# Kernel optimization log

Hardware: AMD Instinct MI355X
Metric: run time of the kernel (lower is better)

The kernel has to match this reference:

```python
import jax, jax.numpy as jnp
import numpy as np

L, B, D, H = 2048, 2, 1024, 16
HD = D // H
DFF = 4 * D
EPS = 1e-5


def layernorm(x, g, b):
    mu = jnp.mean(x, axis=-1, keepdims=True)
    var = jnp.mean((x - mu) ** 2, axis=-1, keepdims=True)
    return (x - mu) * jax.lax.rsqrt(var + EPS) * g + b


def setup_inputs() -> dict:
    key = jax.random.key(0)
    ks = jax.random.split(key, 12)
    s = 0.02
    return {
        "x": jax.random.normal(ks[0], (L, B, D), jnp.float32),
        "ln1_g": jnp.ones((D,), jnp.float32),
        "ln1_b": jnp.zeros((D,), jnp.float32),
        "w_attn": jax.random.normal(ks[1], (D, 3 * D), jnp.float32) * s,
        "b_attn": jnp.zeros((3 * D,), jnp.float32),
        "w_proj": jax.random.normal(ks[2], (D, D), jnp.float32) * s,
        "b_proj": jnp.zeros((D,), jnp.float32),
        "ln2_g": jnp.ones((D,), jnp.float32),
        "ln2_b": jnp.zeros((D,), jnp.float32),
        "w_fc": jax.random.normal(ks[3], (D, DFF), jnp.float32) * s,
        "b_fc": jnp.zeros((DFF,), jnp.float32),
        "w_out": jax.random.normal(ks[4], (DFF, D), jnp.float32) * s,
        "b_out": jnp.zeros((D,), jnp.float32),
    }


def reference(x, ln1_g, ln1_b, w_attn, b_attn, w_proj, b_proj,
              ln2_g, ln2_b, w_fc, b_fc, w_out, b_out):
    # x: [L, B, D]
    h = layernorm(x, ln1_g, ln1_b)
    qkv = h @ w_attn + b_attn                     # [L, B, 3D]
    qkv = jnp.transpose(qkv, (1, 0, 2))            # [B, L, 3D]
    q, k, v = jnp.split(qkv, 3, axis=-1)

    def split_heads(t):                            # [B, L, D] -> [B, H, L, hd]
        return jnp.transpose(t.reshape(B, L, H, HD), (0, 2, 1, 3))

    q, k, v = split_heads(q), split_heads(k), split_heads(v)
    # present: stack of (key, value), key in [B,H,L,hd] layout (post transpose-back)
    present = jnp.stack((k, v))                    # [2, B, H, L, hd]

    scores = jnp.einsum('bhqd,bhkd->bhqk', q, k) / jnp.sqrt(jnp.float32(HD))
    w = jax.nn.softmax(scores, axis=-1)
    a = jnp.einsum('bhqk,bhkd->bhqd', w, v)        # [B, H, L, hd]
    a = jnp.transpose(a, (0, 2, 1, 3)).reshape(B, L, D)
    a = a @ w_proj + b_proj                        # [B, L, D]
    a = jnp.transpose(a, (1, 0, 2))                # [L, B, D]

    x = x + a
    m = jax.nn.gelu(layernorm(x, ln2_g, ln2_b) @ w_fc + b_fc) @ w_out + b_out
    x = x + m
    return x, present
```

## Files before the change

### kernel.cpp

```cpp
#include <hip/hip_runtime.h>
#include <stdint.h>

#define L_SEQ 2048
#define BATCH 2
#define DIM   1024
#define NH    16
#define HDIM  64
#define DFF_  4096
#define ROWS  (L_SEQ*BATCH)

#define QSCALE 0.18033688011112042f

typedef __attribute__((ext_vector_type(8))) short  bf16x8;
typedef __attribute__((ext_vector_type(4))) float  floatx4;

__device__ __forceinline__ unsigned short f2bf(float f) {
    union { float f; uint32_t u; } x; x.f = f;
    uint32_t r = x.u + 0x7fffu + ((x.u >> 16) & 1u);
    return (unsigned short)(r >> 16);
}
__device__ __forceinline__ float bf2f(unsigned short b) {
    union { uint32_t u; float f; } x; x.u = ((uint32_t)b) << 16;
    return x.f;
}
__device__ __forceinline__ uint32_t fbits(float f) {
    union { float f; uint32_t u; } x; x.f = f; return x.u;
}

__device__ __forceinline__ void load_lds16(const unsigned short* g, unsigned short* l) {
    __builtin_amdgcn_global_load_lds(
        (const __attribute__((address_space(1))) unsigned int*)g,
        (__attribute__((address_space(3))) unsigned int*)l, 16, 0, 0);
}

__global__ __launch_bounds__(256)
void transpose_all(const float* __restrict__ s0, unsigned short* __restrict__ d0,
                   const float* __restrict__ s1, unsigned short* __restrict__ d1,
                   const float* __restrict__ s2, unsigned short* __restrict__ d2,
                   const float* __restrict__ s3, unsigned short* __restrict__ d3)
{
    const int id = blockIdx.x;
    const float* src; unsigned short* dst; int K, N, local;
    if (id < 3072)      { src = s0; dst = d0; K = 1024; N = 3072; local = id; }
    else if (id < 4096) { src = s1; dst = d1; K = 1024; N = 1024; local = id - 3072; }
    else if (id < 8192) { src = s2; dst = d2; K = 1024; N = 4096; local = id - 4096; }
    else                { src = s3; dst = d3; K = 4096; N = 1024; local = id - 8192; }
    const int nN = N >> 5;
    const int bk = (local / nN) * 32, bn = (local % nN) * 32;

    __shared__ float tile[32][36];
    const int t = threadIdx.x;
    const int r = t >> 3, c4 = (t & 7) * 4;
    *(float4*)&tile[r][c4] = *(const float4*)(src + (size_t)(bk + r) * N + bn + c4);
    __syncthreads();
    ushort4 o;
    o.x = f2bf(tile[c4 + 0][r]);
    o.y = f2bf(tile[c4 + 1][r]);
    o.z = f2bf(tile[c4 + 2][r]);
    o.w = f2bf(tile[c4 + 3][r]);
    *(ushort4*)(dst + (size_t)(bn + r) * K + bk + c4) = o;
}

template<int INBF16>
__global__ __launch_bounds__(256)
void ln_rows(const void* __restrict__ xin, const float* __restrict__ g,
             const float* __restrict__ bta, unsigned short* __restrict__ out)
{
    const int row = blockIdx.x;
    const int t = threadIdx.x;
    float4 v;
    if (INBF16) {
        const ushort4 u = ((const ushort4*)((const unsigned short*)xin + (size_t)row * DIM))[t];
        v.x = bf2f(u.x); v.y = bf2f(u.y); v.z = bf2f(u.z); v.w = bf2f(u.w);
    } else {
        v = ((const float4*)((const float*)xin + (size_t)row * DIM))[t];
    }
    float s  = v.x + v.y + v.z + v.w;
    float s2 = v.x*v.x + v.y*v.y + v.z*v.z + v.w*v.w;
#pragma unroll
    for (int d = 1; d < 64; d <<= 1) { s += __shfl_xor(s, d, 64); s2 += __shfl_xor(s2, d, 64); }
    __shared__ float ss[4], ss2[4];
    const int w = t >> 6, lane = t & 63;
    if (lane == 0) { ss[w] = s; ss2[w] = s2; }
    __syncthreads();
    s  = ss[0] + ss[1] + ss[2] + ss[3];
    s2 = ss2[0] + ss2[1] + ss2[2] + ss2[3];
    const float mu   = s * (1.0f / DIM);
    const float var  = s2 * (1.0f / DIM) - mu * mu;
    const float rstd = rsqrtf(var + 1e-5f);
    const float4 gv = ((const float4*)g)[t];
    const float4 bv = ((const float4*)bta)[t];
    ushort4 o;
    o.x = f2bf((v.x - mu) * rstd * gv.x + bv.x);
    o.y = f2bf((v.y - mu) * rstd * gv.y + bv.y);
    o.z = f2bf((v.z - mu) * rstd * gv.z + bv.z);
    o.w = f2bf((v.w - mu) * rstd * gv.w + bv.w);
    *(ushort4*)(out + (size_t)row * DIM + t * 4) = o;
}

template<int GELU, int RESID, int OUTBF16, int MI>
__global__ __launch_bounds__(256)
void gemm_bt(const unsigned short* __restrict__ A,
             const unsigned short* __restrict__ Bt,
             const float* __restrict__ bias,
             const void* __restrict__ resid,
             void* __restrict__ outp,
             int M, int N, int K)
{
    __shared__ unsigned short As[MI * 32 * 32];
    __shared__ unsigned short Bs[128 * 32];
    const int t = threadIdx.x;
    const int w = t >> 6, lane = t & 63;
    const int quad = lane >> 4, l16 = lane & 15;
    const int wm = (w >> 1) * (MI * 16), wn = (w & 1) * 64;
    const int bm = blockIdx.x * (MI * 32), bn = blockIdx.y * 128;

    const int srow = lane >> 2;
    const int scol = (lane & 3) * 8;

    const unsigned short* Ab = A  + (size_t)bm * K;
    const unsigned short* Bb = Bt + (size_t)bn * K;

    floatx4 acc[MI][4] = {};

    for (int kc = 0; kc < K; kc += 32) {
        __syncthreads();
#pragma unroll
        for (int i = 0; i < MI / 2; ++i) {
            const int r0 = (i * 4 + w) * 16;
            load_lds16(Ab + (size_t)(r0 + srow) * K + kc + scol, As + r0 * 32);
        }
#pragma unroll
        for (int i = 0; i < 2; ++i) {
            const int r0 = (i * 4 + w) * 16;
            load_lds16(Bb + (size_t)(r0 + srow) * K + kc + scol, Bs + r0 * 32);
        }
        __syncthreads();
        bf16x8 af[MI], bf[4];
#pragma unroll
        for (int i = 0; i < MI; ++i) af[i] = *(const bf16x8*)(As + (wm + i*16 + l16) * 32 + quad * 8);
#pragma unroll
        for (int j = 0; j < 4; ++j) bf[j] = *(const bf16x8*)(Bs + (wn + j*16 + l16) * 32 + quad * 8);
#pragma unroll
        for (int i = 0; i < MI; ++i)
#pragma unroll
            for (int j = 0; j < 4; ++j)
                acc[i][j] = __builtin_amdgcn_mfma_f32_16x16x32_bf16(af[i], bf[j], acc[i][j], 0, 0, 0);
    }

#pragma unroll
    for (int i = 0; i < MI; ++i) {
#pragma unroll
        for (int j = 0; j < 4; ++j) {
            const int col = bn + wn + j*16 + l16;
            const float bv = bias[col];
#pragma unroll
            for (int r = 0; r < 4; ++r) {
                const int row = bm + wm + i*16 + quad*4 + r;
                float v = acc[i][j][r] + bv;
                if (RESID == 1) v += ((const float*)resid)[(size_t)row * N + col];
                if (RESID == 2) v += bf2f(((const unsigned short*)resid)[(size_t)row * N + col]);
                if (GELU) {
                    const float u = v;
                    const float c = 0.7978845608028654f * (u + 0.044715f * u * u * u);
                    v = 0.5f * u * (1.0f + tanhf(c));
                }
                if (OUTBF16) ((unsigned short*)outp)[(size_t)row * N + col] = f2bf(v);
                else         ((float*)outp)[(size_t)row * N + col] = v;
            }
        }
    }
}

__global__ __launch_bounds__(256)
void split_qkv(const unsigned short* __restrict__ qkv,
               unsigned short* __restrict__ q, unsigned short* __restrict__ k,
               float* __restrict__ present)
{
    const size_t idx = (size_t)blockIdx.x * 256 + threadIdx.x;
    const int g8  = idx & 7;
    const int l   = (idx >> 3) & 2047;
    const int bh  = (idx >> 14) & 31;
    const int sel = (int)(idx >> 19);
    const int b = bh >> 4, h = bh & 15;
    const unsigned short* src = qkv + (size_t)(l * BATCH + b) * (3 * DIM) + sel * DIM + h * HDIM + g8 * 8;
    const uint4 val = *(const uint4*)src;
    const unsigned short* sv = (const unsigned short*)&val;
    if (sel == 0) {
        unsigned short ov[8];
#pragma unroll
        for (int j = 0; j < 8; ++j) ov[j] = f2bf(bf2f(sv[j]) * QSCALE);
        *(uint4*)(q + ((size_t)bh * L_SEQ + l) * HDIM + g8 * 8) = *(uint4*)ov;
    } else {
        *(uint4*)(k + ((size_t)bh * L_SEQ + l) * HDIM + g8 * 8) = val;
        float* p = present + (((size_t)b * NH + h) * L_SEQ + l) * HDIM + (size_t)g8 * 8;
        float4 f0, f1;
        f0.x = bf2f(sv[0]); f0.y = bf2f(sv[1]); f0.z = bf2f(sv[2]); f0.w = bf2f(sv[3]);
        f1.x = bf2f(sv[4]); f1.y = bf2f(sv[5]); f1.z = bf2f(sv[6]); f1.w = bf2f(sv[7]);
        ((float4*)p)[0] = f0; ((float4*)p)[1] = f1;
    }
}

__global__ __launch_bounds__(256)
void transpose_v(const unsigned short* __restrict__ qkv, unsigned short* __restrict__ vt,
                 float* __restrict__ present)
{
    __shared__ unsigned short tile[64][72];
    const int lt = blockIdx.x;
    const int bh = blockIdx.y;
    const int b = bh >> 4, h = bh & 15;
    const int t = threadIdx.x;
#pragma unroll
    for (int i = 0; i < 2; ++i) {
        const int idx = i * 256 + t;
        const int l = idx >> 3, c = (idx & 7) * 8;
        const uint4 val =
            *(const uint4*)(qkv + (size_t)((lt * 64 + l) * BATCH + b) * (3 * DIM) + 2 * DIM + h * HDIM + c);
        *(uint4*)(&tile[l][c]) = val;
        const unsigned short* sv = (const unsigned short*)&val;
        float* p = present + ((((size_t)BATCH + b) * NH + h) * L_SEQ + lt * 64 + l) * HDIM + c;
        float4 f0, f1;
        f0.x = bf2f(sv[0]); f0.y = bf2f(sv[1]); f0.z = bf2f(sv[2]); f0.w = bf2f(sv[3]);
        f1.x = bf2f(sv[4]); f1.y = bf2f(sv[5]); f1.z = bf2f(sv[6]); f1.w = bf2f(sv[7]);
        ((float4*)p)[0] = f0; ((float4*)p)[1] = f1;
    }
    __syncthreads();
#pragma unroll
    for (int i = 0; i < 2; ++i) {
        const int idx = i * 256 + t;
        const int d = idx >> 3, l0 = (idx & 7) * 8;
        const int kk = l0 >> 3;
        ushort4 o[2];
        unsigned short* ov = (unsigned short*)o;
#pragma unroll
        for (int jj = 0; jj < 8; ++jj) {
            const int j = (jj + kk) & 7;
            ov[j] = tile[l0 + j][d];
        }
        *(uint4*)(vt + ((size_t)bh * HDIM + d) * L_SEQ + lt * 64 + l0) = *(uint4*)o;
    }
}

__global__ __launch_bounds__(256)
void attn_kernel(const unsigned short* __restrict__ Q,
                 const unsigned short* __restrict__ Kk,
                 const unsigned short* __restrict__ Vt,
                 unsigned short* __restrict__ Aout)
{
    const int qt = blockIdx.x;
    const int bh = blockIdx.y;
    const int b = bh >> 4, h = bh & 15;
    const int t = threadIdx.x, w = t >> 6, lane = t & 63;
    const int quad = lane >> 4, l16 = lane & 15;

    __shared__ unsigned short Ks[64][72];
    __shared__ unsigned short Vts[64][72];
    __shared__ unsigned short Ps[4][32][72];

    const size_t head_off = (size_t)bh * L_SEQ * HDIM;
    const int q_base = qt * 128 + w * 32;

    bf16x8 qf[2][2];
#pragma unroll
    for (int nf = 0; nf < 2; ++nf)
#pragma unroll
        for (int ds = 0; ds < 2; ++ds)
            qf[nf][ds] = *(const bf16x8*)(Q + head_off + (size_t)(q_base + nf*16 + l16) * HDIM + ds*32 + quad*8);

    floatx4 o[4][2] = {};
    float l_i[2] = {0.f, 0.f};

    for (int kt = 0; kt < L_SEQ; kt += 64) {
        __syncthreads();
#pragma unroll
        for (int i = 0; i < 2; ++i) {
            const int idx = i * 256 + t;
            const int row = idx >> 3, col = (idx & 7) * 8;
            *(uint4*)(&Ks[row][col])  = *(const uint4*)(Kk + head_off + (size_t)(kt + row) * HDIM + col);
            *(uint4*)(&Vts[row][col]) = *(const uint4*)(Vt + head_off + (size_t)row * L_SEQ + kt + col);
        }
        __syncthreads();

        floatx4 s[4][2] = {};
#pragma unroll
        for (int ds = 0; ds < 2; ++ds)
#pragma unroll
            for (int jt = 0; jt < 4; ++jt) {
                const bf16x8 kf = *(const bf16x8*)(&Ks[jt*16 + l16][ds*32 + quad*8]);
                s[jt][0] = __builtin_amdgcn_mfma_f32_16x16x32_bf16(kf, qf[0][ds], s[jt][0], 0, 0, 0);
                s[jt][1] = __builtin_amdgcn_mfma_f32_16x16x32_bf16(kf, qf[1][ds], s[jt][1], 0, 0, 0);
            }

#pragma unroll
        for (int nf = 0; nf < 2; ++nf) {
#pragma unroll
            for (int jt = 0; jt < 4; ++jt) {
                const float p0 = exp2f(s[jt][nf][0]);
                const float p1 = exp2f(s[jt][nf][1]);
                const float p2 = exp2f(s[jt][nf][2]);
                const float p3 = exp2f(s[jt][nf][3]);
                l_i[nf] += (p0 + p1) + (p2 + p3);
                uint2 pk;
                pk.x = __builtin_amdgcn_perm(fbits(p1), fbits(p0), 0x07060302u);
                pk.y = __builtin_amdgcn_perm(fbits(p3), fbits(p2), 0x07060302u);
                *(uint2*)(&Ps[w][nf*16 + l16][jt*16 + quad*4]) = pk;
            }
        }

#pragma unroll
        for (int ks = 0; ks < 2; ++ks) {
            const bf16x8 pf0 = *(const bf16x8*)(&Ps[w][l16]     [ks*32 + quad*8]);
            const bf16x8 pf1 = *(const bf16x8*)(&Ps[w][16 + l16][ks*32 + quad*8]);
#pragma unroll
            for (int dt = 0; dt < 4; ++dt) {
                const bf16x8 vf = *(const bf16x8*)(&Vts[dt*16 + l16][ks*32 + quad*8]);
                o[dt][0] = __builtin_amdgcn_mfma_f32_16x16x32_bf16(vf, pf0, o[dt][0], 0, 0, 0);
                o[dt][1] = __builtin_amdgcn_mfma_f32_16x16x32_bf16(vf, pf1, o[dt][1], 0, 0, 0);
            }
        }
    }

#pragma unroll
    for (int nf = 0; nf < 2; ++nf) {
        float l = l_i[nf];
        l += __shfl_xor(l, 16, 64);
        l += __shfl_xor(l, 32, 64);
        const float inv = 1.0f / l;
        const int row = q_base + nf*16 + l16;
#pragma unroll
        for (int dt = 0; dt < 4; ++dt) {
            ushort4 ov;
            ov.x = f2bf(o[dt][nf][0] * inv); ov.y = f2bf(o[dt][nf][1] * inv);
            ov.z = f2bf(o[dt][nf][2] * inv); ov.w = f2bf(o[dt][nf][3] * inv);
            *(ushort4*)(Aout + (size_t)(row * BATCH + b) * DIM + h * HDIM + dt*16 + quad*4) = ov;
        }
    }
}

extern "C" void kernel_launch(void* const* d_in, const int* in_sizes, int n_in,
                              void* d_out, int out_size, void* d_ws, size_t ws_size,
                              hipStream_t stream)
{
    const float* x      = (const float*)d_in[0];
    const float* ln1_g  = (const float*)d_in[1];
    const float* ln1_b  = (const float*)d_in[2];
    const float* w_attn = (const float*)d_in[3];
    const float* b_attn = (const float*)d_in[4];
    const float* w_proj = (const float*)d_in[5];
    const float* b_proj = (const float*)d_in[6];
    const float* ln2_g  = (const float*)d_in[7];
    const float* ln2_b  = (const float*)d_in[8];
    const float* w_fc   = (const float*)d_in[9];
    const float* b_fc   = (const float*)d_in[10];
    const float* w_out  = (const float*)d_in[11];
    const float* b_out  = (const float*)d_in[12];

    char* ws = (char*)d_ws;
    unsigned short* watT   = (unsigned short*)(ws + 0);
    unsigned short* wprojT = (unsigned short*)(ws + 6291456);
    unsigned short* wfcT   = (unsigned short*)(ws + 8388608);
    unsigned short* woutT  = (unsigned short*)(ws + 16777216);
    unsigned short* h      = (unsigned short*)(ws + 25165824);
    unsigned short* qkv    = (unsigned short*)(ws + 33554432);
    unsigned short* mws    = (unsigned short*)(ws + 33554432);
    unsigned short* qw     = (unsigned short*)(ws + 58720256);
    unsigned short* kw     = (unsigned short*)(ws + 67108864);
    unsigned short* vt     = (unsigned short*)(ws + 75497472);
    unsigned short* aw     = (unsigned short*)(ws + 83886080);
    unsigned short* x2     = (unsigned short*)(ws + 92274688);

    float* xout    = (float*)d_out;
    float* present = (float*)d_out + 4194304;

    transpose_all<<<12288, 256, 0, stream>>>(w_attn, watT, w_proj, wprojT, w_fc, wfcT, w_out, woutT);

    ln_rows<0><<<ROWS, 256, 0, stream>>>(x, ln1_g, ln1_b, h);
    gemm_bt<0,0,1,4><<<dim3(32, 24), 256, 0, stream>>>(h, watT, b_attn, nullptr, qkv, ROWS, 3*DIM, DIM);
    split_qkv<<<4096, 256, 0, stream>>>(qkv, qw, kw, present);
    transpose_v<<<dim3(32, 32), 256, 0, stream>>>(qkv, vt, present);
    attn_kernel<<<dim3(16, 32), 256, 0, stream>>>(qw, kw, vt, aw);
    gemm_bt<0,1,1,2><<<dim3(64, 8), 256, 0, stream>>>(aw, wprojT, b_proj, x, x2, ROWS, DIM, DIM);
    ln_rows<1><<<ROWS, 256, 0, stream>>>(x2, ln2_g, ln2_b, h);
    gemm_bt<1,0,1,4><<<dim3(32, 32), 256, 0, stream>>>(h, wfcT, b_fc, nullptr, mws, ROWS, DFF_, DIM);
    gemm_bt<0,2,0,2><<<dim3(64, 8), 256, 0, stream>>>(mws, woutT, b_out, x2, xout, ROWS, DIM, DFF_);
}
```

Before: 460.6 us.

## Shrink attention query tile, prefetch K/V into registers, use exp2-based GELU

Each attention block now covers 64 queries instead of 128, one 16-row fragment per wave, which doubles the grid to 1024 blocks for more parallelism. The next K/V tile is loaded into registers while the current one is in shared memory, overlapping global loads with MFMA work. Each K/V tile load is now reused by half as many queries, so total K/V traffic doubles. GELU's tanh is rewritten as a sigmoid computed with exp2 to save ALU work in the FC GEMM epilogue.

```diff
diff --git a/kernel.cpp b/kernel.cpp
--- a/kernel.cpp
+++ b/kernel.cpp
@@ -162,8 +162,10 @@
                 if (RESID == 2) v += bf2f(((const unsigned short*)resid)[(size_t)row * N + col]);
                 if (GELU) {
                     const float u = v;
-                    const float c = 0.7978845608028654f * (u + 0.044715f * u * u * u);
-                    v = 0.5f * u * (1.0f + tanhf(c));
+                    float c = 2.302204225929898f * (u + 0.044715f * u * u * u);
+                    c = fminf(c, 80.f);
+                    const float e = exp2f(c);
+                    v = u * (e / (1.0f + e));
                 }
                 if (OUTBF16) ((unsigned short*)outp)[(size_t)row * N + col] = f2bf(v);
                 else         ((float*)outp)[(size_t)row * N + col] = v;
@@ -255,85 +257,92 @@
 
     __shared__ unsigned short Ks[64][72];
     __shared__ unsigned short Vts[64][72];
-    __shared__ unsigned short Ps[4][32][72];
+    __shared__ unsigned short Ps[4][16][72];
 
     const size_t head_off = (size_t)bh * L_SEQ * HDIM;
-    const int q_base = qt * 128 + w * 32;
-
-    bf16x8 qf[2][2];
-#pragma unroll
-    for (int nf = 0; nf < 2; ++nf)
-#pragma unroll
-        for (int ds = 0; ds < 2; ++ds)
-            qf[nf][ds] = *(const bf16x8*)(Q + head_off + (size_t)(q_base + nf*16 + l16) * HDIM + ds*32 + quad*8);
-
-    floatx4 o[4][2] = {};
-    float l_i[2] = {0.f, 0.f};
+    const int q0 = qt * 64 + w * 16;
+
+    bf16x8 qf[2];
+#pragma unroll
+    for (int ds = 0; ds < 2; ++ds)
+        qf[ds] = *(const bf16x8*)(Q + head_off + (size_t)(q0 + l16) * HDIM + ds*32 + quad*8);
+
+    const int sr0 = t >> 3;
+    const int sc  = (t & 7) * 8;
+
+    uint4 kr[2], vr[2];
+#pragma unroll
+    for (int i = 0; i < 2; ++i) {
+        const int row = sr0 + i * 32;
+        kr[i] = *(const uint4*)(Kk + head_off + (size_t)row * HDIM + sc);
+        vr[i] = *(const uint4*)(Vt + head_off + (size_t)row * L_SEQ + sc);
+    }
+
+    floatx4 o[4] = {};
+    float l_i = 0.f;
 
     for (int kt = 0; kt < L_SEQ; kt += 64) {
         __syncthreads();
 #pragma unroll
         for (int i = 0; i < 2; ++i) {
-            const int idx = i * 256 + t;
-            const int row = idx >> 3, col = (idx & 7) * 8;
-            *(uint4*)(&Ks[row][col])  = *(const uint4*)(Kk + head_off + (size_t)(kt + row) * HDIM + col);
-            *(uint4*)(&Vts[row][col]) = *(const uint4*)(Vt + head_off + (size_t)row * L_SEQ + kt + col);
+            const int row = sr0 + i * 32;
+            *(uint4*)(&Ks[row][sc])  = kr[i];
+            *(uint4*)(&Vts[row][sc]) = vr[i];
+        }
+        if (kt + 64 < L_SEQ) {
+#pragma unroll
+            for (int i = 0; i < 2; ++i) {
+                const int row = sr0 + i * 32;
+                kr[i] = *(const uint4*)(Kk + head_off + (size_t)(kt + 64 + row) * HDIM + sc);
+                vr[i] = *(const uint4*)(Vt + head_off + (size_t)row * L_SEQ + kt + 64 + sc);
+            }
         }
         __syncthreads();
 
-        floatx4 s[4][2] = {};
+        floatx4 s[4] = {};
 #pragma unroll
         for (int ds = 0; ds < 2; ++ds)
 #pragma unroll
             for (int jt = 0; jt < 4; ++jt) {
                 const bf16x8 kf = *(const bf16x8*)(&Ks[jt*16 + l16][ds*32 + quad*8]);
-                s[jt][0] = __builtin_amdgcn_mfma_f32_16x16x32_bf16(kf, qf[0][ds], s[jt][0], 0, 0, 0);
-                s[jt][1] = __builtin_amdgcn_mfma_f32_16x16x32_bf16(kf, qf[1][ds], s[jt][1], 0, 0, 0);
+                s[jt] = __builtin_amdgcn_mfma_f32_16x16x32_bf16(kf, qf[ds], s[jt], 0, 0, 0);
             }
 
 #pragma unroll
-        for (int nf = 0; nf < 2; ++nf) {
-#pragma unroll
-            for (int jt = 0; jt < 4; ++jt) {
-                const float p0 = exp2f(s[jt][nf][0]);
-                const float p1 = exp2f(s[jt][nf][1]);
-                const float p2 = exp2f(s[jt][nf][2]);
-                const float p3 = exp2f(s[jt][nf][3]);
-                l_i[nf] += (p0 + p1) + (p2 + p3);
-                uint2 pk;
-                pk.x = __builtin_amdgcn_perm(fbits(p1), fbits(p0), 0x07060302u);
-                pk.y = __builtin_amdgcn_perm(fbits(p3), fbits(p2), 0x07060302u);
-                *(uint2*)(&Ps[w][nf*16 + l16][jt*16 + quad*4]) = pk;
-            }
+        for (int jt = 0; jt < 4; ++jt) {
+            const float p0 = exp2f(s[jt][0]);
+            const float p1 = exp2f(s[jt][1]);
+            const float p2 = exp2f(s[jt][2]);
+            const float p3 = exp2f(s[jt][3]);
+            l_i += (p0 + p1) + (p2 + p3);
+            uint2 pk;
+            pk.x = __builtin_amdgcn_perm(fbits(p1), fbits(p0), 0x07060302u);
+            pk.y = __builtin_amdgcn_perm(fbits(p3), fbits(p2), 0x07060302u);
+            *(uint2*)(&Ps[w][l16][jt*16 + quad*4]) = pk;
         }
 
 #pragma unroll
         for (int ks = 0; ks < 2; ++ks) {
-            const bf16x8 pf0 = *(const bf16x8*)(&Ps[w][l16]     [ks*32 + quad*8]);
-            const bf16x8 pf1 = *(const bf16x8*)(&Ps[w][16 + l16][ks*32 + quad*8]);
+            const bf16x8 pf = *(const bf16x8*)(&Ps[w][l16][ks*32 + quad*8]);
 #pragma unroll
             for (int dt = 0; dt < 4; ++dt) {
                 const bf16x8 vf = *(const bf16x8*)(&Vts[dt*16 + l16][ks*32 + quad*8]);
-                o[dt][0] = __builtin_amdgcn_mfma_f32_16x16x32_bf16(vf, pf0, o[dt][0], 0, 0, 0);
-                o[dt][1] = __builtin_amdgcn_mfma_f32_16x16x32_bf16(vf, pf1, o[dt][1], 0, 0, 0);
+                o[dt] = __builtin_amdgcn_mfma_f32_16x16x32_bf16(vf, pf, o[dt], 0, 0, 0);
             }
         }
     }
 
-#pragma unroll
-    for (int nf = 0; nf < 2; ++nf) {
-        float l = l_i[nf];
-        l += __shfl_xor(l, 16, 64);
-        l += __shfl_xor(l, 32, 64);
-        const float inv = 1.0f / l;
-        const int row = q_base + nf*16 + l16;
-#pragma unroll
-        for (int dt = 0; dt < 4; ++dt) {
-            ushort4 ov;
-            ov.x = f2bf(o[dt][nf][0] * inv); ov.y = f2bf(o[dt][nf][1] * inv);
-            ov.z = f2bf(o[dt][nf][2] * inv); ov.w = f2bf(o[dt][nf][3] * inv);
-            *(ushort4*)(Aout + (size_t)(row * BATCH + b) * DIM + h * HDIM + dt*16 + quad*4) = ov;
-        }
+    float l = l_i;
+    l += __shfl_xor(l, 16, 64);
+    l += __shfl_xor(l, 32, 64);
+    const float inv = 1.0f / l;
+    const int row = q0 + l16;
+#pragma unroll
+    for (int dt = 0; dt < 4; ++dt) {
+        ushort4 ov;
+        ov.x = f2bf(o[dt][0] * inv); ov.y = f2bf(o[dt][1] * inv);
+        ov.z = f2bf(o[dt][2] * inv); ov.w = f2bf(o[dt][3] * inv);
+        *(ushort4*)(Aout + (size_t)(row * BATCH + b) * DIM + h * HDIM + dt*16 + quad*4) = ov;
     }
 }
 
@@ -378,7 +387,7 @@
     gemm_bt<0,0,1,4><<<dim3(32, 24), 256, 0, stream>>>(h, watT, b_attn, nullptr, qkv, ROWS, 3*DIM, DIM);
     split_qkv<<<4096, 256, 0, stream>>>(qkv, qw, kw, present);
     transpose_v<<<dim3(32, 32), 256, 0, stream>>>(qkv, vt, present);
-    attn_kernel<<<dim3(16, 32), 256, 0, stream>>>(qw, kw, vt, aw);
+    attn_kernel<<<dim3(32, 32), 256, 0, stream>>>(qw, kw, vt, aw);
     gemm_bt<0,1,1,2><<<dim3(64, 8), 256, 0, stream>>>(aw, wprojT, b_proj, x, x2, ROWS, DIM, DIM);
     ln_rows<1><<<ROWS, 256, 0, stream>>>(x2, ln2_g, ln2_b, h);
     gemm_bt<1,0,1,4><<<dim3(32, 32), 256, 0, stream>>>(h, wfcT, b_fc, nullptr, mws, ROWS, DFF_, DIM);
```

New measurement: 512.3 us. 11.2% more time.
